# Performance work log

Hardware: AMD Instinct MI355X
Metric: run time of the kernel (lower is better)

The kernel has to match this reference:

```python
import jax, jax.numpy as jnp
import numpy as np

N, E, IN_DIM, HID, NUM_CLASSES = 100000, 1600000, 256, 128, 40


def setup_inputs() -> dict:
    key = jax.random.key(0)
    ks = jax.random.split(key, 16)
    f32 = jnp.float32

    def w(k, shape):
        fan_in = shape[0]
        return (jax.random.normal(k, shape, f32) / jnp.sqrt(jnp.asarray(fan_in, f32)))

    x = jax.random.normal(ks[0], (N, IN_DIM), f32)
    edge_index = jax.random.randint(ks[1], (2, E), 0, N, dtype=jnp.int32)
    adj_embed = jax.random.normal(ks[2], (N, HID), f32) * 0.02  # xavier-ish
    return {
        "x": x,
        "edge_index": edge_index,
        "adj_embed": adj_embed,
        "wx1": w(ks[3], (IN_DIM, HID)), "bx1": jnp.zeros((HID,), f32),
        "wx2": w(ks[4], (HID, HID)),    "bx2": jnp.zeros((HID,), f32),
        "wa1": w(ks[5], (HID, HID)),    "ba1": jnp.zeros((HID,), f32),
        "wa2": w(ks[6], (HID, HID)),    "ba2": jnp.zeros((HID,), f32),
        "ww1": w(ks[7], (2 * HID, HID)), "bw1": jnp.zeros((HID,), f32),
        "wc": w(ks[8], (HID, NUM_CLASSES)), "bc": jnp.zeros((NUM_CLASSES,), f32),
    }


def _aggregate_neighbours(edge_index, weights, num_nodes):
    src, dst = edge_index[0], edge_index[1]
    # scatter-sum of gathered rows [E, HID] into [num_nodes, HID]
    agg = jax.ops.segment_sum(weights[src], dst, num_segments=num_nodes)
    deg = jax.ops.segment_sum(jnp.ones_like(dst, dtype=weights.dtype), dst,
                              num_segments=num_nodes)
    deg = jnp.maximum(deg, 1.0)[:, None]
    return agg / deg


def reference(x, edge_index, adj_embed, wx1, bx1, wx2, bx2,
              wa1, ba1, wa2, ba2, ww1, bw1, wc, bc):
    # mlp_x (dropout = identity in eval mode)
    hx = jax.nn.relu(x @ wx1 + bx1) @ wx2 + bx2          # [N, HID]
    # adjacency branch: mean-aggregate learned node embeddings over edges
    ha_raw = _aggregate_neighbours(edge_index, adj_embed, adj_embed.shape[0])
    ha = jax.nn.relu(ha_raw @ wa1 + ba1) @ wa2 + ba2     # [N, HID]
    # mlp_w over concat (num_layers=1 -> single Linear+ReLU)
    combined = jnp.concatenate([hx, ha], axis=1)         # [N, 2*HID]
    h = jax.nn.relu(combined @ ww1 + bw1)                # [N, HID]
    h = jax.nn.relu(h + hx + ha)
    logits = h @ wc + bc                                 # [N, NUM_CLASSES]
    return logits
```

## Files before the change

kernel.cpp:

```cpp
#include <hip/hip_runtime.h>

#define Nn 100000
#define Ee 1600000
#define IND 256
#define HD 128
#define NCLS 40
#define NBLK 391

typedef _Float16 f16;
typedef f16 f16x8 __attribute__((ext_vector_type(8)));
typedef f16 f16x4 __attribute__((ext_vector_type(4)));
typedef float f32x4 __attribute__((ext_vector_type(4)));

extern "C" __global__ void __launch_bounds__(256)
k_prep(const float* __restrict__ wx1, const float* __restrict__ wx2,
       const float* __restrict__ wa1, const float* __restrict__ wa2,
       const float* __restrict__ ww1, const float* __restrict__ wc,
       f16* __restrict__ wp,
       const float* __restrict__ emb, f16* __restrict__ embh,
       const int* __restrict__ ei, int* __restrict__ counts,
       int* __restrict__ rank) {
    int bid = blockIdx.x;
    int t = threadIdx.x;
    if (bid < 1563) {
        int e0 = bid * 1024 + t;
#pragma unroll
        for (int k = 0; k < 4; k++) {
            int e = e0 + k * 256;
            if (e < Ee) {
                int dst = ei[Ee + e];
                rank[e] = atomicAdd(&counts[dst], 1);
            }
        }
        return;
    }
    if (bid < 7813) {
        int i = (bid - 1563) * 256 + t;
        const float4* pp = (const float4*)emb + (size_t)i * 2;
        float4 a = pp[0], b = pp[1];
        f16x8 h;
        h[0] = (f16)a.x; h[1] = (f16)a.y; h[2] = (f16)a.z; h[3] = (f16)a.w;
        h[4] = (f16)b.x; h[5] = (f16)b.y; h[6] = (f16)b.z; h[7] = (f16)b.w;
        *(f16x8*)(embh + (size_t)i * 8) = h;
        return;
    }
    int idx = (bid - 7813) * 256 + t;
    const float* W;
    int K, base;
    if (idx < 32768)       { W = wx1; K = 256; base = 0; }
    else if (idx < 49152)  { W = wx2; K = 128; base = 32768; }
    else if (idx < 65536)  { W = wa1; K = 128; base = 49152; }
    else if (idx < 81920)  { W = wa2; K = 128; base = 65536; }
    else if (idx < 114688) { W = ww1; K = 256; base = 81920; }
    else {
        int local = idx - 114688;
        int j = local & 7;
        int L = (local >> 3) & 63;
        int kt = (local >> 9) & 3;
        int ft = local / 2048;
        int k = kt * 32 + (L >> 4) * 8 + j;
        int n = ft * 16 + (L & 15);
        wp[idx] = (n < NCLS) ? (f16)wc[k * NCLS + n] : (f16)0.f;
        return;
    }
    int local = idx - base;
    int KT = K >> 5;
    int j = local & 7;
    int L = (local >> 3) & 63;
    int kt = (local >> 9) % KT;
    int ft = local / (512 * KT);
    int k = kt * 32 + (L >> 4) * 8 + j;
    int n = ft * 16 + (L & 15);
    wp[idx] = (f16)W[k * HD + n];
}

extern "C" __global__ void __launch_bounds__(256)
k_scan1(const int* __restrict__ counts, int* __restrict__ bsum) {
    __shared__ int s[256];
    int t = threadIdx.x;
    int i = blockIdx.x * 256 + t;
    s[t] = (i < Nn) ? counts[i] : 0;
    __syncthreads();
    for (int d = 128; d > 0; d >>= 1) {
        if (t < d) s[t] += s[t + d];
        __syncthreads();
    }
    if (t == 0) bsum[blockIdx.x] = s[0];
}

extern "C" __global__ void __launch_bounds__(256)
k_scan3(const int* __restrict__ counts, const int* __restrict__ bsum,
        int* __restrict__ offsets) {
    __shared__ int s[256];
    __shared__ int basev;
    int t = threadIdx.x;
    int i = blockIdx.x * 256 + t;
    int partial = 0;
    for (int k = t; k < blockIdx.x; k += 256) partial += bsum[k];
    s[t] = partial;
    __syncthreads();
    for (int d = 128; d > 0; d >>= 1) {
        if (t < d) s[t] += s[t + d];
        __syncthreads();
    }
    if (t == 0) basev = s[0];
    __syncthreads();
    int v = (i < Nn) ? counts[i] : 0;
    s[t] = v;
    __syncthreads();
    for (int d = 1; d < 256; d <<= 1) {
        int x = (t >= d) ? s[t - d] : 0;
        __syncthreads();
        s[t] += x;
        __syncthreads();
    }
    if (i < Nn) offsets[i] = basev + s[t] - v;
    if (i == 0) offsets[Nn] = Ee;
}

extern "C" __global__ void __launch_bounds__(256)
k_scatter2(const int* __restrict__ ei, const int* __restrict__ offsets,
           const int* __restrict__ rank, int* __restrict__ bucket) {
    int e = blockIdx.x * 256 + threadIdx.x;
    int dst = ei[Ee + e];
    bucket[offsets[dst] + rank[e]] = ei[e];
}

extern "C" __global__ void __launch_bounds__(256)
k_gather(const int* __restrict__ offsets, const int* __restrict__ bucket,
         const f16* __restrict__ embh, f16* __restrict__ harawp) {
    int t = threadIdx.x;
    int lane = t & 63;
    int node = blockIdx.x * 4 + (t >> 6);
    int q = lane >> 4;
    int cl = (lane & 15) * 8;

    int beg = offsets[node];
    int end = offsets[node + 1];
    int deg = end - beg;

    int myidx = (lane < deg) ? bucket[beg + lane] : 0;

    float s[8];
#pragma unroll
    for (int j = 0; j < 8; j++) s[j] = 0.f;

    int dlim = (deg < 64) ? deg : 64;
    int e = q;
    for (; e + 4 < dlim; e += 8) {
        int a0 = __shfl(myidx, e);
        int a1 = __shfl(myidx, e + 4);
        f16x8 v0 = *(const f16x8*)(embh + (size_t)a0 * HD + cl);
        f16x8 v1 = *(const f16x8*)(embh + (size_t)a1 * HD + cl);
#pragma unroll
        for (int j = 0; j < 8; j++) s[j] += (float)v0[j] + (float)v1[j];
    }
    if (e < dlim) {
        int a0 = __shfl(myidx, e);
        f16x8 v0 = *(const f16x8*)(embh + (size_t)a0 * HD + cl);
#pragma unroll
        for (int j = 0; j < 8; j++) s[j] += (float)v0[j];
    }
    for (int i = beg + 64 + q; i < end; i += 4) {
        int a0 = bucket[i];
        f16x8 v0 = *(const f16x8*)(embh + (size_t)a0 * HD + cl);
#pragma unroll
        for (int j = 0; j < 8; j++) s[j] += (float)v0[j];
    }

#pragma unroll
    for (int j = 0; j < 8; j++) {
        s[j] += __shfl_down(s[j], 32);
        s[j] += __shfl_down(s[j], 16);
    }

    if (lane < 16) {
        float inv = 1.0f / fmaxf((float)deg, 1.0f);
        f16x8 h;
#pragma unroll
        for (int j = 0; j < 8; j++) h[j] = (f16)(s[j] * inv);
        int nt = node >> 4, m = node & 15;
        int kt = lane >> 2, q2 = lane & 3;
        *(f16x8*)(harawp + (((nt * 4 + kt) * 64 + m + 16 * q2) * 8)) = h;
    }
}

extern "C" __global__ void __launch_bounds__(256, 6)
linkx_mlp(const float* __restrict__ x, const f16* __restrict__ harawp,
          const f16* __restrict__ wx1p, const float* __restrict__ bx1,
          const f16* __restrict__ wx2p, const float* __restrict__ bx2,
          const f16* __restrict__ wa1p, const float* __restrict__ ba1,
          const f16* __restrict__ wa2p, const float* __restrict__ ba2,
          const f16* __restrict__ ww1p, const float* __restrict__ bw1,
          const f16* __restrict__ wcp, const float* __restrict__ bc,
          float* __restrict__ out) {
    __shared__ __align__(16) f16 shr[4096];
    __shared__ __align__(16) f16 hxp[4096];
    __shared__ __align__(16) f16 hap[4096];

    const int t = threadIdx.x;
    const int node0 = blockIdx.x * 32;
    const int lane = t & 63;
    const int wid = t >> 6;
    const int mt = wid >> 1;
    const int fh = wid & 1;

    f32x4 acc[4];
    float rreg[4][4];

#define INIT_ACC(BIAS)                                                    \
    _Pragma("unroll")                                                     \
    for (int q = 0; q < 4; q++) {                                         \
        float bv = (BIAS)[(fh * 4 + q) * 16 + (lane & 15)];               \
        acc[q][0] = bv; acc[q][1] = bv; acc[q][2] = bv; acc[q][3] = bv;   \
    }

#define GEMM_K128(APACK, BP)                                                  \
    _Pragma("unroll")                                                         \
    for (int kt = 0; kt < 4; kt++) {                                          \
        f16x8 a = *(const f16x8*)((APACK) + ((mt * 4 + kt) * 64 + lane) * 8); \
        _Pragma("unroll")                                                     \
        for (int q = 0; q < 4; q++) {                                         \
            f16x8 b = *(const f16x8*)((BP) + (((fh*4+q)*4 + kt)*64 + lane)*8);\
            acc[q] = __builtin_amdgcn_mfma_f32_16x16x32_f16(a, b, acc[q], 0, 0, 0); \
        }                                                                     \
    }

#define EPILOGUE(MODE, PDST)                                                  \
    _Pragma("unroll")                                                         \
    for (int q = 0; q < 4; q++) {                                             \
        int f = (fh * 4 + q) * 16 + (lane & 15);                              \
        int kt2 = f >> 5, q2 = (f >> 3) & 3, j2 = f & 7;                      \
        _Pragma("unroll")                                                     \
        for (int r = 0; r < 4; r++) {                                         \
            int n = (lane >> 4) * 4 + r;                                      \
            float v = acc[q][r];                                              \
            if (MODE == 0) v = fmaxf(v, 0.f);                                 \
            if (MODE == 1) rreg[q][r] = v;                                    \
            if (MODE == 2) rreg[q][r] += v;                                   \
            if (MODE == 3) v = fmaxf(fmaxf(v, 0.f) + rreg[q][r], 0.f);        \
            (PDST)[((mt * 4 + kt2) * 64 + n + 16 * q2) * 8 + j2] = (f16)v;    \
        }                                                                     \
    }

    INIT_ACC(bx1)
    {
        const float* xbase = x + (size_t)(node0 + mt * 16 + (lane & 15)) * IND
                               + (lane >> 4) * 8;
        float4 u[16];
#pragma unroll
        for (int kt = 0; kt < 8; kt++) {
            u[2 * kt]     = *(const float4*)(xbase + kt * 32);
            u[2 * kt + 1] = *(const float4*)(xbase + kt * 32 + 4);
        }
#pragma unroll
        for (int kt = 0; kt < 8; kt++) {
            float4 u0 = u[2 * kt], u1 = u[2 * kt + 1];
            f16x8 a;
            a[0] = (f16)u0.x; a[1] = (f16)u0.y; a[2] = (f16)u0.z; a[3] = (f16)u0.w;
            a[4] = (f16)u1.x; a[5] = (f16)u1.y; a[6] = (f16)u1.z; a[7] = (f16)u1.w;
#pragma unroll
            for (int q = 0; q < 4; q++) {
                f16x8 b = *(const f16x8*)(wx1p + (((fh*4+q)*8 + kt)*64 + lane)*8);
                acc[q] = __builtin_amdgcn_mfma_f32_16x16x32_f16(a, b, acc[q], 0, 0, 0);
            }
        }
    }
    EPILOGUE(0, shr)
    __syncthreads();

    INIT_ACC(bx2)
    GEMM_K128(shr, wx2p)
    EPILOGUE(1, hxp)
    __syncthreads();

    INIT_ACC(ba1)
    {
        int ntb = (node0 >> 4) + mt;
        f16x8 av[4];
#pragma unroll
        for (int kt = 0; kt < 4; kt++)
            av[kt] = *(const f16x8*)(harawp + ((ntb * 4 + kt) * 64 + lane) * 8);
#pragma unroll
        for (int kt = 0; kt < 4; kt++) {
#pragma unroll
            for (int q = 0; q < 4; q++) {
                f16x8 b = *(const f16x8*)(wa1p + (((fh*4+q)*4 + kt)*64 + lane)*8);
                acc[q] = __builtin_amdgcn_mfma_f32_16x16x32_f16(av[kt], b, acc[q], 0, 0, 0);
            }
        }
    }
    EPILOGUE(0, shr)
    __syncthreads();

    INIT_ACC(ba2)
    GEMM_K128(shr, wa2p)
    EPILOGUE(2, hap)
    __syncthreads();

    INIT_ACC(bw1)
#pragma unroll
    for (int kt = 0; kt < 8; kt++) {
        const f16* ap = (kt < 4) ? (hxp + ((mt * 4 + kt) * 64 + lane) * 8)
                                 : (hap + ((mt * 4 + (kt - 4)) * 64 + lane) * 8);
        f16x8 a = *(const f16x8*)ap;
#pragma unroll
        for (int q = 0; q < 4; q++) {
            f16x8 b = *(const f16x8*)(ww1p + (((fh*4+q)*8 + kt)*64 + lane)*8);
            acc[q] = __builtin_amdgcn_mfma_f32_16x16x32_f16(a, b, acc[q], 0, 0, 0);
        }
    }
    EPILOGUE(3, shr)
    __syncthreads();

    {
        int nft = (fh == 0) ? 2 : 1;
#pragma unroll 2
        for (int ii = 0; ii < nft; ii++) {
            int ft = (ii == 0) ? fh : 2;
            int f = ft * 16 + (lane & 15);
            f32x4 c;
            float bv = (f < NCLS) ? bc[f] : 0.f;
            c[0] = bv; c[1] = bv; c[2] = bv; c[3] = bv;
#pragma unroll
            for (int kt = 0; kt < 4; kt++) {
                f16x8 a = *(const f16x8*)(shr + ((mt * 4 + kt) * 64 + lane) * 8);
                f16x8 b = *(const f16x8*)(wcp + ((ft * 4 + kt) * 64 + lane) * 8);
                c = __builtin_amdgcn_mfma_f32_16x16x32_f16(a, b, c, 0, 0, 0);
            }
            if (f < NCLS) {
#pragma unroll
                for (int r = 0; r < 4; r++) {
                    int n = node0 + mt * 16 + (lane >> 4) * 4 + r;
                    out[(size_t)n * NCLS + f] = c[r];
                }
            }
        }
    }
}

extern "C" void kernel_launch(void* const* d_in, const int* in_sizes, int n_in,
                              void* d_out, int out_size, void* d_ws, size_t ws_size,
                              hipStream_t stream) {
    const float* x   = (const float*)d_in[0];
    const int*   ei  = (const int*)d_in[1];
    const float* emb = (const float*)d_in[2];
    const float* wx1 = (const float*)d_in[3];
    const float* bx1 = (const float*)d_in[4];
    const float* wx2 = (const float*)d_in[5];
    const float* bx2 = (const float*)d_in[6];
    const float* wa1 = (const float*)d_in[7];
    const float* ba1 = (const float*)d_in[8];
    const float* wa2 = (const float*)d_in[9];
    const float* ba2 = (const float*)d_in[10];
    const float* ww1 = (const float*)d_in[11];
    const float* bw1 = (const float*)d_in[12];
    const float* wc  = (const float*)d_in[13];
    const float* bc  = (const float*)d_in[14];
    float* out = (float*)d_out;

    int* ws = (int*)d_ws;
    int* counts  = ws;
    int* offsets = ws + 2 * Nn;
    int* bsum    = ws + 3 * Nn + 16;
    int* bucket  = ws + 3 * Nn + 512;
    f16* wp      = (f16*)(ws + 3 * Nn + 512 + Ee);
    f16* wx1p = wp;
    f16* wx2p = wp + 32768;
    f16* wa1p = wp + 49152;
    f16* wa2p = wp + 65536;
    f16* ww1p = wp + 81920;
    f16* wcp  = wp + 114688;
    f16* harawp = wp + 131072;
    f16* embh   = harawp + (size_t)Nn * HD;
    int* rank = (int*)harawp;

    hipMemsetAsync(ws, 0, (size_t)Nn * sizeof(int), stream);

    k_prep<<<8285, 256, 0, stream>>>(wx1, wx2, wa1, wa2, ww1, wc, wp,
                                     emb, embh, ei, counts, rank);
    k_scan1<<<NBLK, 256, 0, stream>>>(counts, bsum);
    k_scan3<<<NBLK, 256, 0, stream>>>(counts, bsum, offsets);
    k_scatter2<<<Ee / 256, 256, 0, stream>>>(ei, offsets, rank, bucket);
    k_gather<<<Nn / 4, 256, 0, stream>>>(offsets, bucket, embh, harawp);

    linkx_mlp<<<Nn / 32, 256, 0, stream>>>(x, harawp,
                                           wx1p, bx1, wx2p, bx2,
                                           wa1p, ba1, wa2p, ba2,
                                           ww1p, bw1, wcp, bc, out);
}
```

Baseline: 479.8 us.

## Move x-branch MLP into prep kernel to overlap with edge counting

Splits weight packing into its own kernel and moves the hx = MLP(x) computation into the prep kernel as extra blocks, so it runs concurrently with the atomic degree counting and embedding conversion instead of after aggregation. hx is written to global memory in packed fp16 and re-read by the final MLP kernel, which loses that shared buffer and changes launch bounds from 6 to 4 waves. It adds an extra kernel launch and global round-trip for hx, and the residual now uses fp16-rounded hx.

```diff
diff --git a/kernel.cpp b/kernel.cpp
--- a/kernel.cpp
+++ b/kernel.cpp
@@ -9,42 +9,48 @@
 
 typedef _Float16 f16;
 typedef f16 f16x8 __attribute__((ext_vector_type(8)));
-typedef f16 f16x4 __attribute__((ext_vector_type(4)));
 typedef float f32x4 __attribute__((ext_vector_type(4)));
 
-extern "C" __global__ void __launch_bounds__(256)
-k_prep(const float* __restrict__ wx1, const float* __restrict__ wx2,
-       const float* __restrict__ wa1, const float* __restrict__ wa2,
-       const float* __restrict__ ww1, const float* __restrict__ wc,
-       f16* __restrict__ wp,
-       const float* __restrict__ emb, f16* __restrict__ embh,
-       const int* __restrict__ ei, int* __restrict__ counts,
-       int* __restrict__ rank) {
-    int bid = blockIdx.x;
-    int t = threadIdx.x;
-    if (bid < 1563) {
-        int e0 = bid * 1024 + t;
-#pragma unroll
-        for (int k = 0; k < 4; k++) {
-            int e = e0 + k * 256;
-            if (e < Ee) {
-                int dst = ei[Ee + e];
-                rank[e] = atomicAdd(&counts[dst], 1);
-            }
-        }
-        return;
-    }
-    if (bid < 7813) {
-        int i = (bid - 1563) * 256 + t;
-        const float4* pp = (const float4*)emb + (size_t)i * 2;
-        float4 a = pp[0], b = pp[1];
-        f16x8 h;
-        h[0] = (f16)a.x; h[1] = (f16)a.y; h[2] = (f16)a.z; h[3] = (f16)a.w;
-        h[4] = (f16)b.x; h[5] = (f16)b.y; h[6] = (f16)b.z; h[7] = (f16)b.w;
-        *(f16x8*)(embh + (size_t)i * 8) = h;
-        return;
-    }
-    int idx = (bid - 7813) * 256 + t;
+#define INIT_ACC(BIAS)                                                    \
+    _Pragma("unroll")                                                     \
+    for (int q = 0; q < 4; q++) {                                         \
+        float bv = (BIAS)[(fh * 4 + q) * 16 + (lane & 15)];               \
+        acc[q][0] = bv; acc[q][1] = bv; acc[q][2] = bv; acc[q][3] = bv;   \
+    }
+
+#define GEMM_K128(APACK, BP)                                                  \
+    _Pragma("unroll")                                                         \
+    for (int kt = 0; kt < 4; kt++) {                                          \
+        f16x8 a = *(const f16x8*)((APACK) + ((mt * 4 + kt) * 64 + lane) * 8); \
+        _Pragma("unroll")                                                     \
+        for (int q = 0; q < 4; q++) {                                         \
+            f16x8 b = *(const f16x8*)((BP) + (((fh*4+q)*4 + kt)*64 + lane)*8);\
+            acc[q] = __builtin_amdgcn_mfma_f32_16x16x32_f16(a, b, acc[q], 0, 0, 0); \
+        }                                                                     \
+    }
+
+#define EPILOGUE(MODE, PDST)                                                  \
+    _Pragma("unroll")                                                         \
+    for (int q = 0; q < 4; q++) {                                             \
+        int f = (fh * 4 + q) * 16 + (lane & 15);                              \
+        int kt2 = f >> 5, q2 = (f >> 3) & 3, j2 = f & 7;                      \
+        _Pragma("unroll")                                                     \
+        for (int r = 0; r < 4; r++) {                                         \
+            int n = (lane >> 4) * 4 + r;                                      \
+            float v = acc[q][r];                                              \
+            if (MODE == 0) v = fmaxf(v, 0.f);                                 \
+            if (MODE == 2) rreg[q][r] += v;                                   \
+            if (MODE == 3) v = fmaxf(fmaxf(v, 0.f) + rreg[q][r], 0.f);        \
+            (PDST)[((mt * 4 + kt2) * 64 + n + 16 * q2) * 8 + j2] = (f16)v;    \
+        }                                                                     \
+    }
+
+extern "C" __global__ void __launch_bounds__(256)
+k_wpack(const float* __restrict__ wx1, const float* __restrict__ wx2,
+        const float* __restrict__ wa1, const float* __restrict__ wa2,
+        const float* __restrict__ ww1, const float* __restrict__ wc,
+        f16* __restrict__ wp) {
+    int idx = blockIdx.x * 256 + threadIdx.x;
     const float* W;
     int K, base;
     if (idx < 32768)       { W = wx1; K = 256; base = 0; }
@@ -75,6 +81,92 @@
 }
 
 extern "C" __global__ void __launch_bounds__(256)
+k_prep(const int* __restrict__ ei, int* __restrict__ counts,
+       int* __restrict__ rank,
+       const float* __restrict__ emb, f16* __restrict__ embh,
+       const float* __restrict__ x,
+       const f16* __restrict__ wx1p, const float* __restrict__ bx1,
+       const f16* __restrict__ wx2p, const float* __restrict__ bx2,
+       f16* __restrict__ hxp) {
+    __shared__ __align__(16) f16 pshr[4096];
+    int bid = blockIdx.x;
+    int t = threadIdx.x;
+    if (bid < 1563) {
+        int e0 = bid * 1024 + t;
+#pragma unroll
+        for (int k = 0; k < 4; k++) {
+            int e = e0 + k * 256;
+            if (e < Ee) {
+                int dst = ei[Ee + e];
+                rank[e] = atomicAdd(&counts[dst], 1);
+            }
+        }
+        return;
+    }
+    if (bid < 7813) {
+        int i = (bid - 1563) * 256 + t;
+        const float4* pp = (const float4*)emb + (size_t)i * 2;
+        float4 a = pp[0], b = pp[1];
+        f16x8 h;
+        h[0] = (f16)a.x; h[1] = (f16)a.y; h[2] = (f16)a.z; h[3] = (f16)a.w;
+        h[4] = (f16)b.x; h[5] = (f16)b.y; h[6] = (f16)b.z; h[7] = (f16)b.w;
+        *(f16x8*)(embh + (size_t)i * 8) = h;
+        return;
+    }
+    int unit = bid - 7813;
+    const int node0 = unit * 32;
+    const int lane = t & 63;
+    const int wid = t >> 6;
+    const int mt = wid >> 1;
+    const int fh = wid & 1;
+    f32x4 acc[4];
+    float rreg[4][4];
+    (void)rreg;
+
+    INIT_ACC(bx1)
+    {
+        const float* xbase = x + (size_t)(node0 + mt * 16 + (lane & 15)) * IND
+                               + (lane >> 4) * 8;
+        float4 u[16];
+#pragma unroll
+        for (int kt = 0; kt < 8; kt++) {
+            u[2 * kt]     = *(const float4*)(xbase + kt * 32);
+            u[2 * kt + 1] = *(const float4*)(xbase + kt * 32 + 4);
+        }
+#pragma unroll
+        for (int kt = 0; kt < 8; kt++) {
+            float4 u0 = u[2 * kt], u1 = u[2 * kt + 1];
+            f16x8 a;
+            a[0] = (f16)u0.x; a[1] = (f16)u0.y; a[2] = (f16)u0.z; a[3] = (f16)u0.w;
+            a[4] = (f16)u1.x; a[5] = (f16)u1.y; a[6] = (f16)u1.z; a[7] = (f16)u1.w;
+#pragma unroll
+            for (int q = 0; q < 4; q++) {
+                f16x8 b = *(const f16x8*)(wx1p + (((fh*4+q)*8 + kt)*64 + lane)*8);
+                acc[q] = __builtin_amdgcn_mfma_f32_16x16x32_f16(a, b, acc[q], 0, 0, 0);
+            }
+        }
+    }
+    EPILOGUE(0, pshr)
+    __syncthreads();
+
+    INIT_ACC(bx2)
+    GEMM_K128(pshr, wx2p)
+    {
+        int gnt = unit * 2 + mt;
+#pragma unroll
+        for (int q = 0; q < 4; q++) {
+            int f = (fh * 4 + q) * 16 + (lane & 15);
+            int kt2 = f >> 5, q2 = (f >> 3) & 3, j2 = f & 7;
+#pragma unroll
+            for (int r = 0; r < 4; r++) {
+                int n = (lane >> 4) * 4 + r;
+                hxp[((gnt * 4 + kt2) * 64 + n + 16 * q2) * 8 + j2] = (f16)acc[q][r];
+            }
+        }
+    }
+}
+
+extern "C" __global__ void __launch_bounds__(256)
 k_scan1(const int* __restrict__ counts, int* __restrict__ bsum) {
     __shared__ int s[256];
     int t = threadIdx.x;
@@ -185,17 +277,14 @@
     }
 }
 
-extern "C" __global__ void __launch_bounds__(256, 6)
-linkx_mlp(const float* __restrict__ x, const f16* __restrict__ harawp,
-          const f16* __restrict__ wx1p, const float* __restrict__ bx1,
-          const f16* __restrict__ wx2p, const float* __restrict__ bx2,
+extern "C" __global__ void __launch_bounds__(256, 4)
+linkx_mlp(const f16* __restrict__ harawp, const f16* __restrict__ hxp,
           const f16* __restrict__ wa1p, const float* __restrict__ ba1,
           const f16* __restrict__ wa2p, const float* __restrict__ ba2,
           const f16* __restrict__ ww1p, const float* __restrict__ bw1,
           const f16* __restrict__ wcp, const float* __restrict__ bc,
           float* __restrict__ out) {
     __shared__ __align__(16) f16 shr[4096];
-    __shared__ __align__(16) f16 hxp[4096];
     __shared__ __align__(16) f16 hap[4096];
 
     const int t = threadIdx.x;
@@ -204,83 +293,29 @@
     const int wid = t >> 6;
     const int mt = wid >> 1;
     const int fh = wid & 1;
+    const int gntb = (node0 >> 4) + mt;
 
     f32x4 acc[4];
     float rreg[4][4];
 
-#define INIT_ACC(BIAS)                                                    \
-    _Pragma("unroll")                                                     \
-    for (int q = 0; q < 4; q++) {                                         \
-        float bv = (BIAS)[(fh * 4 + q) * 16 + (lane & 15)];               \
-        acc[q][0] = bv; acc[q][1] = bv; acc[q][2] = bv; acc[q][3] = bv;   \
-    }
-
-#define GEMM_K128(APACK, BP)                                                  \
-    _Pragma("unroll")                                                         \
-    for (int kt = 0; kt < 4; kt++) {                                          \
-        f16x8 a = *(const f16x8*)((APACK) + ((mt * 4 + kt) * 64 + lane) * 8); \
-        _Pragma("unroll")                                                     \
-        for (int q = 0; q < 4; q++) {                                         \
-            f16x8 b = *(const f16x8*)((BP) + (((fh*4+q)*4 + kt)*64 + lane)*8);\
-            acc[q] = __builtin_amdgcn_mfma_f32_16x16x32_f16(a, b, acc[q], 0, 0, 0); \
-        }                                                                     \
-    }
-
-#define EPILOGUE(MODE, PDST)                                                  \
-    _Pragma("unroll")                                                         \
-    for (int q = 0; q < 4; q++) {                                             \
-        int f = (fh * 4 + q) * 16 + (lane & 15);                              \
-        int kt2 = f >> 5, q2 = (f >> 3) & 3, j2 = f & 7;                      \
-        _Pragma("unroll")                                                     \
-        for (int r = 0; r < 4; r++) {                                         \
-            int n = (lane >> 4) * 4 + r;                                      \
-            float v = acc[q][r];                                              \
-            if (MODE == 0) v = fmaxf(v, 0.f);                                 \
-            if (MODE == 1) rreg[q][r] = v;                                    \
-            if (MODE == 2) rreg[q][r] += v;                                   \
-            if (MODE == 3) v = fmaxf(fmaxf(v, 0.f) + rreg[q][r], 0.f);        \
-            (PDST)[((mt * 4 + kt2) * 64 + n + 16 * q2) * 8 + j2] = (f16)v;    \
-        }                                                                     \
-    }
-
-    INIT_ACC(bx1)
-    {
-        const float* xbase = x + (size_t)(node0 + mt * 16 + (lane & 15)) * IND
-                               + (lane >> 4) * 8;
-        float4 u[16];
-#pragma unroll
-        for (int kt = 0; kt < 8; kt++) {
-            u[2 * kt]     = *(const float4*)(xbase + kt * 32);
-            u[2 * kt + 1] = *(const float4*)(xbase + kt * 32 + 4);
-        }
-#pragma unroll
-        for (int kt = 0; kt < 8; kt++) {
-            float4 u0 = u[2 * kt], u1 = u[2 * kt + 1];
-            f16x8 a;
-            a[0] = (f16)u0.x; a[1] = (f16)u0.y; a[2] = (f16)u0.z; a[3] = (f16)u0.w;
-            a[4] = (f16)u1.x; a[5] = (f16)u1.y; a[6] = (f16)u1.z; a[7] = (f16)u1.w;
-#pragma unroll
-            for (int q = 0; q < 4; q++) {
-                f16x8 b = *(const f16x8*)(wx1p + (((fh*4+q)*8 + kt)*64 + lane)*8);
-                acc[q] = __builtin_amdgcn_mfma_f32_16x16x32_f16(a, b, acc[q], 0, 0, 0);
-            }
-        }
-    }
-    EPILOGUE(0, shr)
-    __syncthreads();
-
-    INIT_ACC(bx2)
-    GEMM_K128(shr, wx2p)
-    EPILOGUE(1, hxp)
-    __syncthreads();
+    f16 hxr[4][4];
+#pragma unroll
+    for (int q = 0; q < 4; q++) {
+        int f = (fh * 4 + q) * 16 + (lane & 15);
+        int kt2 = f >> 5, q2 = (f >> 3) & 3, j2 = f & 7;
+#pragma unroll
+        for (int r = 0; r < 4; r++) {
+            int n = (lane >> 4) * 4 + r;
+            hxr[q][r] = hxp[((gntb * 4 + kt2) * 64 + n + 16 * q2) * 8 + j2];
+        }
+    }
 
     INIT_ACC(ba1)
     {
-        int ntb = (node0 >> 4) + mt;
         f16x8 av[4];
 #pragma unroll
         for (int kt = 0; kt < 4; kt++)
-            av[kt] = *(const f16x8*)(harawp + ((ntb * 4 + kt) * 64 + lane) * 8);
+            av[kt] = *(const f16x8*)(harawp + ((gntb * 4 + kt) * 64 + lane) * 8);
 #pragma unroll
         for (int kt = 0; kt < 4; kt++) {
 #pragma unroll
@@ -293,6 +328,11 @@
     EPILOGUE(0, shr)
     __syncthreads();
 
+#pragma unroll
+    for (int q = 0; q < 4; q++)
+#pragma unroll
+        for (int r = 0; r < 4; r++) rreg[q][r] = (float)hxr[q][r];
+
     INIT_ACC(ba2)
     GEMM_K128(shr, wa2p)
     EPILOGUE(2, hap)
@@ -300,10 +340,17 @@
 
     INIT_ACC(bw1)
 #pragma unroll
-    for (int kt = 0; kt < 8; kt++) {
-        const f16* ap = (kt < 4) ? (hxp + ((mt * 4 + kt) * 64 + lane) * 8)
-                                 : (hap + ((mt * 4 + (kt - 4)) * 64 + lane) * 8);
-        f16x8 a = *(const f16x8*)ap;
+    for (int kt = 0; kt < 4; kt++) {
+        f16x8 a = *(const f16x8*)(hxp + ((gntb * 4 + kt) * 64 + lane) * 8);
+#pragma unroll
+        for (int q = 0; q < 4; q++) {
+            f16x8 b = *(const f16x8*)(ww1p + (((fh*4+q)*8 + kt)*64 + lane)*8);
+            acc[q] = __builtin_amdgcn_mfma_f32_16x16x32_f16(a, b, acc[q], 0, 0, 0);
+        }
+    }
+#pragma unroll
+    for (int kt = 4; kt < 8; kt++) {
+        f16x8 a = *(const f16x8*)(hap + ((mt * 4 + (kt - 4)) * 64 + lane) * 8);
 #pragma unroll
         for (int q = 0; q < 4; q++) {
             f16x8 b = *(const f16x8*)(ww1p + (((fh*4+q)*8 + kt)*64 + lane)*8);
@@ -373,19 +420,20 @@
     f16* wcp  = wp + 114688;
     f16* harawp = wp + 131072;
     f16* embh   = harawp + (size_t)Nn * HD;
+    f16* hxp    = embh + (size_t)Nn * HD;
     int* rank = (int*)harawp;
 
     hipMemsetAsync(ws, 0, (size_t)Nn * sizeof(int), stream);
 
-    k_prep<<<8285, 256, 0, stream>>>(wx1, wx2, wa1, wa2, ww1, wc, wp,
-                                     emb, embh, ei, counts, rank);
+    k_wpack<<<472, 256, 0, stream>>>(wx1, wx2, wa1, wa2, ww1, wc, wp);
+    k_prep<<<10938, 256, 0, stream>>>(ei, counts, rank, emb, embh,
+                                      x, wx1p, bx1, wx2p, bx2, hxp);
     k_scan1<<<NBLK, 256, 0, stream>>>(counts, bsum);
     k_scan3<<<NBLK, 256, 0, stream>>>(counts, bsum, offsets);
     k_scatter2<<<Ee / 256, 256, 0, stream>>>(ei, offsets, rank, bucket);
     k_gather<<<Nn / 4, 256, 0, stream>>>(offsets, bucket, embh, harawp);
 
-    linkx_mlp<<<Nn / 32, 256, 0, stream>>>(x, harawp,
-                                           wx1p, bx1, wx2p, bx2,
+    linkx_mlp<<<Nn / 32, 256, 0, stream>>>(harawp, hxp,
                                            wa1p, ba1, wa2p, ba2,
                                            ww1p, bw1, wcp, bc, out);
 }
```

Result: faster. 462.6 us (-3.6%).
